# Kernel tuning notes

Hardware: AMD Instinct MI355X
Metric: run time of the kernel (lower is better)

The kernel has to match this reference:

```python
import jax, jax.numpy as jnp
import numpy as np

LOG_2PI = float(np.log(2.0 * np.pi))


def setup_inputs() -> dict:
    key = jax.random.key(0)
    k1, k2, k3 = jax.random.split(key, 3)
    N, M, D = 8192, 4096, 784
    samples = jax.random.normal(k1, (N, D), dtype=jnp.float32)
    x = jax.random.normal(k2, (M, D), dtype=jnp.float32)
    # per-feature std, kept away from zero for numerical sanity
    std = jax.random.uniform(k3, (D,), dtype=jnp.float32, minval=0.5, maxval=1.5)
    return {"samples": samples, "x": x, "std": std}


def reference(samples, x, std):
    # Diagonal-Gaussian mixture log-prob:
    #   logp[n, m] = sum_d [ -0.5*((s_nd - x_md)/std_d)^2 - 0.5*log(2*pi) - log(std_d) ]
    # computed via the ||u||^2 + ||v||^2 - 2 u.v identity on std-scaled vectors
    # (mathematically identical to the torch broadcast, without the (N,M,D) tensor).
    N, D = samples.shape
    M = x.shape[0]
    u = samples / std  # (N, D)
    v = x / std        # (M, D)
    sq_dist = (
        jnp.sum(u * u, axis=1)[:, None]
        + jnp.sum(v * v, axis=1)[None, :]
        - 2.0 * jnp.einsum("nd,md->nm", u, v)
    )  # (N, M)
    log_const = -0.5 * D * LOG_2PI - jnp.sum(jnp.log(std))
    log_prob = -0.5 * sq_dist + log_const  # (N, M)
    # logsumexp over mixture components, minus log(M)
    return jax.nn.logsumexp(log_prob, axis=1) - jnp.log(jnp.asarray(M, dtype=samples.dtype))
```

## Files before the change

kernel.cpp:

```cpp
#include <hip/hip_runtime.h>
#include <cstdint>
#include <cstddef>


#define N_ROWS 8192
#define M_ROWS 4096
#define D_DIM  784
#define KPB    896
#define LOG2PI 1.8378770664093453f
#define LOGM   8.317766166719343f

typedef unsigned char u8;
typedef __attribute__((ext_vector_type(8))) int   i32x8;
typedef __attribute__((ext_vector_type(4))) float f32x4;

__device__ __forceinline__ void gld16(const u8* g, u8* l) {
    __builtin_amdgcn_global_load_lds(
        (__attribute__((address_space(1))) void*)(void*)g,
        (__attribute__((address_space(3))) void*)l, 16, 0, 0);
}

__global__ __launch_bounds__(256) void k_prep(const float* __restrict__ samples,
                                              const float* __restrict__ x,
                                              const float* __restrict__ stdv,
                                              u8* __restrict__ dst,
                                              float* __restrict__ norm) {
    const int wid = threadIdx.x >> 6, lane = threadIdx.x & 63;
    const int row = blockIdx.x * 4 + wid;
    const float* src = (row < N_ROWS) ? samples + (size_t)row * D_DIM
                                      : x + (size_t)(row - N_ROWS) * D_DIM;
    unsigned* drow = (unsigned*)(dst + (size_t)row * KPB);
    float sq = 0.f;
#pragma unroll
    for (int i = 0; i < 4; ++i) {
        const int c = lane + 64 * i;
        if (c < 224) {
            unsigned p = 0;
            if (c < 196) {
                float4 s = ((const float4*)src)[c];
                float4 d = ((const float4*)stdv)[c];
                float ux = s.x / d.x, uy = s.y / d.y;
                float uz = s.z / d.z, uw = s.w / d.w;
                p = __builtin_amdgcn_cvt_pk_fp8_f32(ux, uy, 0, false);
                p = __builtin_amdgcn_cvt_pk_fp8_f32(uz, uw, p, true);
                float r0 = __builtin_amdgcn_cvt_f32_fp8(p, 0);
                float r1 = __builtin_amdgcn_cvt_f32_fp8(p, 1);
                float r2 = __builtin_amdgcn_cvt_f32_fp8(p, 2);
                float r3 = __builtin_amdgcn_cvt_f32_fp8(p, 3);
                sq += r0 * r0 + r1 * r1 + r2 * r2 + r3 * r3;
            }
            drow[c] = p;
        }
    }
    for (int m = 32; m; m >>= 1) sq += __shfl_xor(sq, m);
    if (lane == 0) norm[row] = sq;
}

__global__ __launch_bounds__(256) void k_gemm(const u8* __restrict__ U,
                                              const u8* __restrict__ V,
                                              const float* __restrict__ vnorm,
                                              float* __restrict__ pmax,
                                              float* __restrict__ psum) {
    __shared__ __align__(16) char smem[65536];
    float2* part = (float2*)smem;

    const int tid = threadIdx.x;
    const int lane = tid & 63;
    const int wid = tid >> 6;
    const int waveRow = wid >> 1;
    const int waveCol = wid & 1;
    const int bCol = blockIdx.x;
    const int bRow = blockIdx.y;
    const int g = lane >> 4, rl = lane & 15;

    const int srow = lane & 15;
    const int sc16 = lane >> 4;
    const u8* ga[4]; const u8* gb[4]; int loff[4];
#pragma unroll
    for (int t = 0; t < 4; ++t) {
        const int lin = wid * 4 + t, h = lin & 1, R = lin >> 1;
        ga[t] = U + (size_t)(bRow * 128 + R * 16 + srow) * KPB + h * 64 + sc16 * 16;
        gb[t] = V + (size_t)(bCol * 128 + R * 16 + srow) * KPB + h * 64 + sc16 * 16;
        loff[t] = lin * 1024;
    }

    const int fo = (g >> 1) * 1024 + (g & 1) * 512 + rl * 16;
    const int aoff = waveRow * 8192 + fo;
    const int boff = 16384 + waveCol * 8192 + fo;

    f32x4 acc[4][4];
#pragma unroll
    for (int i = 0; i < 4; ++i)
#pragma unroll
        for (int j = 0; j < 4; ++j) acc[i][j] = (f32x4){0.f, 0.f, 0.f, 0.f};

#pragma unroll
    for (int t = 0; t < 4; ++t) gld16(ga[t], (u8*)(smem + loff[t]));
#pragma unroll
    for (int t = 0; t < 4; ++t) gld16(gb[t], (u8*)(smem + 16384 + loff[t]));

#pragma unroll
    for (int kt = 0; kt < 7; ++kt) {
        if (kt < 6) {
            char* nb = smem + ((kt + 1) & 1) * 32768;
            const int k1 = (kt + 1) * 128;
#pragma unroll
            for (int t = 0; t < 4; ++t) gld16(ga[t] + k1, (u8*)(nb + loff[t]));
#pragma unroll
            for (int t = 0; t < 4; ++t) gld16(gb[t] + k1, (u8*)(nb + 16384 + loff[t]));
            __builtin_amdgcn_s_waitcnt(0x0F78);
        } else {
            __builtin_amdgcn_s_waitcnt(0x0F70);
        }
        __builtin_amdgcn_s_barrier();

        const char* base = smem + (kt & 1) * 32768;
        i32x8 a[4], b[4];
#pragma unroll
        for (int i = 0; i < 4; ++i) {
            int4 L = *(const int4*)(base + (aoff + i * 2048));
            int4 H = *(const int4*)(base + (aoff + i * 2048 + 256));
            a[i] = (i32x8){L.x, L.y, L.z, L.w, H.x, H.y, H.z, H.w};
        }
#pragma unroll
        for (int j = 0; j < 4; ++j) {
            int4 L = *(const int4*)(base + (boff + j * 2048));
            int4 H = *(const int4*)(base + (boff + j * 2048 + 256));
            b[j] = (i32x8){L.x, L.y, L.z, L.w, H.x, H.y, H.z, H.w};
        }
#pragma unroll
        for (int i = 0; i < 4; ++i)
#pragma unroll
            for (int j = 0; j < 4; ++j)
                acc[i][j] = __builtin_amdgcn_mfma_scale_f32_16x16x128_f8f6f4(
                    a[i], b[j], acc[i][j], 0 , 0 ,
                    0, 127 , 0, 127 );

        __builtin_amdgcn_s_barrier();
    }
    __syncthreads();

    float vn[4];
#pragma unroll
    for (int j = 0; j < 4; ++j) vn[j] = vnorm[bCol * 128 + waveCol * 64 + j * 16 + rl];

    const int prow0 = waveRow * 64 + g * 4;
    const int pcol = waveCol * 16 + rl;
#pragma unroll
    for (int i = 0; i < 4; ++i) {
#pragma unroll
        for (int rg = 0; rg < 4; ++rg) {
            float w0 = acc[i][0][rg] - 0.5f * vn[0];
            float w1 = acc[i][1][rg] - 0.5f * vn[1];
            float w2 = acc[i][2][rg] - 0.5f * vn[2];
            float w3 = acc[i][3][rg] - 0.5f * vn[3];
            float m = fmaxf(fmaxf(w0, w1), fmaxf(w2, w3));
            float s = __expf(w0 - m) + __expf(w1 - m) + __expf(w2 - m) + __expf(w3 - m);
            part[(prow0 + i * 16 + rg) * 33 + pcol] = make_float2(m, s);
        }
    }
    __syncthreads();
    if (tid < 128) {
        const float2* p = part + tid * 33;
        float m = p[0].x;
#pragma unroll
        for (int c = 1; c < 32; ++c) m = fmaxf(m, p[c].x);
        float s = 0.f;
#pragma unroll
        for (int c = 0; c < 32; ++c) { float2 q = p[c]; s += q.y * __expf(q.x - m); }
        size_t grow = (size_t)(bRow * 128 + tid);
        pmax[grow * 32 + bCol] = m;
        psum[grow * 32 + bCol] = s;
    }
}

__global__ __launch_bounds__(256) void k_final(const float* __restrict__ pmax,
                                               const float* __restrict__ psum,
                                               const float* __restrict__ norm,
                                               const float* __restrict__ stdv,
                                               float* __restrict__ out) {
    __shared__ float wsum[4];
    const int t = threadIdx.x;
    float ls = 0.f;
    for (int d = t; d < D_DIM; d += 256) ls += logf(stdv[d]);
    for (int m = 32; m; m >>= 1) ls += __shfl_xor(ls, m);
    if ((t & 63) == 0) wsum[t >> 6] = ls;
    __syncthreads();
    const float logc = -0.5f * (float)D_DIM * LOG2PI - (wsum[0] + wsum[1] + wsum[2] + wsum[3]);

    const int n = blockIdx.x * 256 + t;
    const float* pm = pmax + (size_t)n * 32;
    const float* ps = psum + (size_t)n * 32;
    float gm = pm[0];
#pragma unroll
    for (int c = 1; c < 32; ++c) gm = fmaxf(gm, pm[c]);
    float S = 0.f;
#pragma unroll
    for (int c = 0; c < 32; ++c) S += ps[c] * __expf(pm[c] - gm);
    out[n] = gm + logf(S) - 0.5f * norm[n] + logc - LOGM;
}

extern "C" void kernel_launch(void* const* d_in, const int* in_sizes, int n_in,
                              void* d_out, int out_size, void* d_ws, size_t ws_size,
                              hipStream_t stream) {
    const float* samples = (const float*)d_in[0];
    const float* x       = (const float*)d_in[1];
    const float* stdv    = (const float*)d_in[2];
    float* out = (float*)d_out;

    char* ws = (char*)d_ws;
    u8*    U    = (u8*)ws;
    u8*    V    = (u8*)(ws + 7340032);
    float* norm = (float*)(ws + 11010048);
    float* pmax = (float*)(ws + 11059200);
    float* psum = (float*)(ws + 12107776);

    k_prep<<<(N_ROWS + M_ROWS) / 4, 256, 0, stream>>>(samples, x, stdv, U, norm);
    k_gemm<<<dim3(M_ROWS / 128, N_ROWS / 128), 256, 0, stream>>>(U, V, norm + N_ROWS, pmax, psum);
    k_final<<<N_ROWS / 256, 256, 0, stream>>>(pmax, psum, norm, stdv, out);
}
```

Before: 149.7 us.

## Stage GEMM tiles through registers with swizzled LDS layout and one barrier

Replaces the direct global-to-LDS loads in the fp8 GEMM with register-staged global loads. Each k-tile is written to LDS with an XOR-style row swizzle, so the later 16-byte fragment reads are meant to avoid bank conflicts. The next tile's global loads are issued right after the current tile's LDS writes, and the trailing per-iteration barrier is dropped, since double buffering already keeps reads and writes apart. This costs extra VGPRs for the staged data plus explicit ds_write instructions, and the wait now covers only LDS operations.

```diff
diff --git a/kernel.cpp b/kernel.cpp
--- a/kernel.cpp
+++ b/kernel.cpp
@@ -13,12 +13,6 @@
 typedef unsigned char u8;
 typedef __attribute__((ext_vector_type(8))) int   i32x8;
 typedef __attribute__((ext_vector_type(4))) float f32x4;
-
-__device__ __forceinline__ void gld16(const u8* g, u8* l) {
-    __builtin_amdgcn_global_load_lds(
-        (__attribute__((address_space(1))) void*)(void*)g,
-        (__attribute__((address_space(3))) void*)l, 16, 0, 0);
-}
 
 __global__ __launch_bounds__(256) void k_prep(const float* __restrict__ samples,
                                               const float* __restrict__ x,
@@ -73,20 +67,26 @@
     const int bRow = blockIdx.y;
     const int g = lane >> 4, rl = lane & 15;
 
-    const int srow = lane & 15;
-    const int sc16 = lane >> 4;
+    const int sr = lane >> 2;
+    const int sc = lane & 3;
+    const int wsub = sc * 256 + (((sr + 4 * sc) & 15) * 16);
     const u8* ga[4]; const u8* gb[4]; int loff[4];
 #pragma unroll
     for (int t = 0; t < 4; ++t) {
         const int lin = wid * 4 + t, h = lin & 1, R = lin >> 1;
-        ga[t] = U + (size_t)(bRow * 128 + R * 16 + srow) * KPB + h * 64 + sc16 * 16;
-        gb[t] = V + (size_t)(bCol * 128 + R * 16 + srow) * KPB + h * 64 + sc16 * 16;
-        loff[t] = lin * 1024;
-    }
-
-    const int fo = (g >> 1) * 1024 + (g & 1) * 512 + rl * 16;
-    const int aoff = waveRow * 8192 + fo;
-    const int boff = 16384 + waveCol * 8192 + fo;
+        ga[t] = U + (size_t)(bRow * 128 + R * 16 + sr) * KPB + h * 64 + sc * 16;
+        gb[t] = V + (size_t)(bCol * 128 + R * 16 + sr) * KPB + h * 64 + sc * 16;
+        loff[t] = lin * 1024 + wsub;
+    }
+
+    const int h = g >> 1;
+    const int cL = 2 * (g & 1), cH = cL + 1;
+    const int foL = h * 1024 + cL * 256 + (((rl + 4 * cL) & 15) * 16);
+    const int foH = h * 1024 + cH * 256 + (((rl + 4 * cH) & 15) * 16);
+    const int aoffL = waveRow * 8192 + foL;
+    const int aoffH = waveRow * 8192 + foH;
+    const int boffL = 16384 + waveCol * 8192 + foL;
+    const int boffH = 16384 + waveCol * 8192 + foH;
 
     f32x4 acc[4][4];
 #pragma unroll
@@ -94,38 +94,42 @@
 #pragma unroll
         for (int j = 0; j < 4; ++j) acc[i][j] = (f32x4){0.f, 0.f, 0.f, 0.f};
 
-#pragma unroll
-    for (int t = 0; t < 4; ++t) gld16(ga[t], (u8*)(smem + loff[t]));
-#pragma unroll
-    for (int t = 0; t < 4; ++t) gld16(gb[t], (u8*)(smem + 16384 + loff[t]));
+    int4 ra[4], rb[4];
+#pragma unroll
+    for (int t = 0; t < 4; ++t) ra[t] = *(const int4*)(ga[t]);
+#pragma unroll
+    for (int t = 0; t < 4; ++t) rb[t] = *(const int4*)(gb[t]);
 
 #pragma unroll
     for (int kt = 0; kt < 7; ++kt) {
+        char* wb = smem + (kt & 1) * 32768;
+#pragma unroll
+        for (int t = 0; t < 4; ++t) *(int4*)(wb + loff[t]) = ra[t];
+#pragma unroll
+        for (int t = 0; t < 4; ++t) *(int4*)(wb + 16384 + loff[t]) = rb[t];
+
         if (kt < 6) {
-            char* nb = smem + ((kt + 1) & 1) * 32768;
             const int k1 = (kt + 1) * 128;
 #pragma unroll
-            for (int t = 0; t < 4; ++t) gld16(ga[t] + k1, (u8*)(nb + loff[t]));
-#pragma unroll
-            for (int t = 0; t < 4; ++t) gld16(gb[t] + k1, (u8*)(nb + 16384 + loff[t]));
-            __builtin_amdgcn_s_waitcnt(0x0F78);
-        } else {
-            __builtin_amdgcn_s_waitcnt(0x0F70);
-        }
+            for (int t = 0; t < 4; ++t) ra[t] = *(const int4*)(ga[t] + k1);
+#pragma unroll
+            for (int t = 0; t < 4; ++t) rb[t] = *(const int4*)(gb[t] + k1);
+        }
+
+        __builtin_amdgcn_s_waitcnt(0xC07F);
         __builtin_amdgcn_s_barrier();
-
         const char* base = smem + (kt & 1) * 32768;
         i32x8 a[4], b[4];
 #pragma unroll
         for (int i = 0; i < 4; ++i) {
-            int4 L = *(const int4*)(base + (aoff + i * 2048));
-            int4 H = *(const int4*)(base + (aoff + i * 2048 + 256));
+            int4 L = *(const int4*)(base + (aoffL + i * 2048));
+            int4 H = *(const int4*)(base + (aoffH + i * 2048));
             a[i] = (i32x8){L.x, L.y, L.z, L.w, H.x, H.y, H.z, H.w};
         }
 #pragma unroll
         for (int j = 0; j < 4; ++j) {
-            int4 L = *(const int4*)(base + (boff + j * 2048));
-            int4 H = *(const int4*)(base + (boff + j * 2048 + 256));
+            int4 L = *(const int4*)(base + (boffL + j * 2048));
+            int4 H = *(const int4*)(base + (boffH + j * 2048));
             b[j] = (i32x8){L.x, L.y, L.z, L.w, H.x, H.y, H.z, H.w};
         }
 #pragma unroll
@@ -135,8 +139,6 @@
                 acc[i][j] = __builtin_amdgcn_mfma_scale_f32_16x16x128_f8f6f4(
                     a[i], b[j], acc[i][j], 0 , 0 ,
                     0, 127 , 0, 127 );
-
-        __builtin_amdgcn_s_barrier();
     }
     __syncthreads();
 
```

Result: no change. 147.1 us (-1.7%).
